# Kernel tuning notes

Hardware: AMD Instinct MI355X
Metric: run time of the kernel (lower is better)

The kernel has to match this reference:

```python
import jax, jax.numpy as jnp
import numpy as np

B, N = 8, 256
IN_F, OUT_F = 64, 64
IN_E, OUT_E = 32, 64  # out_edges must equal out_features (batched matmul constraint)


def setup_inputs() -> dict:
    key = jax.random.key(0)
    ks = jax.random.split(key, 9)
    s = 0.05
    return {
        "A": jax.random.uniform(ks[0], (B, N, N), dtype=jnp.float32),
        "emb_node": jax.random.normal(ks[1], (B, N, IN_F), dtype=jnp.float32),
        "emb_edge": jax.random.normal(ks[2], (B, N, N, IN_E), dtype=jnp.float32),
        "W_node": jax.random.normal(ks[3], (IN_F, OUT_F), dtype=jnp.float32) * s,
        "b_node": jnp.zeros((OUT_F,), dtype=jnp.float32),
        "W_nodes": jax.random.normal(ks[4], (IN_F, OUT_F), dtype=jnp.float32) * s,
        "b_nodes": jnp.zeros((OUT_F,), dtype=jnp.float32),
        "W_edge": jax.random.normal(ks[5], (IN_E, OUT_E), dtype=jnp.float32) * s,
        "b_edge": jnp.zeros((OUT_E,), dtype=jnp.float32),
    }


def reference(A, emb_node, emb_edge, W_node, b_node, W_nodes, b_nodes, W_edge, b_edge):
    # Dense projections (last-axis matmul, like keras Dense)
    node_x = emb_node @ W_node + b_node        # [B,N,F]
    node_sx = emb_node @ W_nodes + b_nodes     # [B,N,F]
    edge_x = emb_edge @ W_edge + b_edge        # [B,N,N,E] (E == F)
    # Fused edge-weighted aggregation: original materializes A[...,None]*edge_x
    # then does a per-channel batched matmul with node_x; same math as:
    #   node_out[b,n,f] = sum_m A[b,n,m] * edge_x[b,n,m,f] * node_x[b,m,f]
    agg = jnp.einsum('bnm,bnmf,bmf->bnf', A, edge_x, node_x)
    node_out = jax.nn.relu(agg) + jax.nn.relu(node_sx)
    edge_out = jax.nn.relu(edge_x)
    return node_out, edge_out
```

## Files before the change

kernel.cpp:

```cpp
#include <hip/hip_runtime.h>

#define BB    8
#define NN    256
#define OUTF  64
#define INE   32

using f4     = __attribute__((ext_vector_type(4))) float;
using f32x4  = __attribute__((ext_vector_type(4))) float;
using bf16x8 = __attribute__((ext_vector_type(8))) short;

__device__ float          g_node_x[BB * NN * OUTF];
__device__ float          g_relu_sx[BB * NN * OUTF];
__device__ unsigned short g_wtb[OUTF * INE];

static __device__ __forceinline__ unsigned short f2bf(float x) {
    unsigned u = __builtin_bit_cast(unsigned, x);
    u += 0x7fffu + ((u >> 16) & 1u);
    return (unsigned short)(u >> 16);
}

static __device__ __forceinline__ bf16x8 cvt8(f4 lo, f4 hi) {
    bf16x8 e;
    e[0] = (short)f2bf(lo.x); e[1] = (short)f2bf(lo.y);
    e[2] = (short)f2bf(lo.z); e[3] = (short)f2bf(lo.w);
    e[4] = (short)f2bf(hi.x); e[5] = (short)f2bf(hi.y);
    e[6] = (short)f2bf(hi.z); e[7] = (short)f2bf(hi.w);
    return e;
}

static __device__ __forceinline__ f4 relu4(f4 v) {
    f4 r;
    r.x = fmaxf(v.x, 0.f); r.y = fmaxf(v.y, 0.f);
    r.z = fmaxf(v.z, 0.f); r.w = fmaxf(v.w, 0.f);
    return r;
}

__global__ __launch_bounds__(256) void node_proj(
    const float* __restrict__ emb_node,
    const float* __restrict__ W1, const float* __restrict__ b1,
    const float* __restrict__ W2, const float* __restrict__ b2,
    const float* __restrict__ W_edge)
{
    __shared__ float sW1[64][64];
    __shared__ float sW2[64][64];
    __shared__ float sE[16][64];

    const int tid = threadIdx.x;

    if (blockIdx.x == 0) {
        const int f  = tid >> 2;
        const int k0 = (tid & 3) * 8;
#pragma unroll
        for (int j = 0; j < 8; ++j)
            g_wtb[f * INE + k0 + j] = f2bf(W_edge[(k0 + j) * OUTF + f]);
    }

    const f4* w1v = (const f4*)W1;
    const f4* w2v = (const f4*)W2;
    f4* s1 = (f4*)&sW1[0][0];
    f4* s2 = (f4*)&sW2[0][0];
#pragma unroll
    for (int i = 0; i < 4; ++i) {
        s1[tid + i * 256] = w1v[tid + i * 256];
        s2[tid + i * 256] = w2v[tid + i * 256];
    }
    const int row0 = blockIdx.x * 16;
    ((f4*)&sE[0][0])[tid] = ((const f4*)(emb_node + row0 * 64))[tid];
    __syncthreads();

    const int s = tid >> 6;
    const int f = tid & 63;
    float a1[4], a2[4];
    const float bb1 = b1[f], bb2 = b2[f];
#pragma unroll
    for (int j = 0; j < 4; ++j) { a1[j] = bb1; a2[j] = bb2; }
#pragma unroll
    for (int k = 0; k < 64; ++k) {
        const float w1 = sW1[k][f];
        const float w2 = sW2[k][f];
#pragma unroll
        for (int j = 0; j < 4; ++j) {
            const float e = sE[s + 4 * j][k];
            a1[j] = fmaf(e, w1, a1[j]);
            a2[j] = fmaf(e, w2, a2[j]);
        }
    }
#pragma unroll
    for (int j = 0; j < 4; ++j) {
        const int row = row0 + s + 4 * j;
        g_node_x[row * 64 + f]  = a1[j];
        g_relu_sx[row * 64 + f] = fmaxf(a2[j], 0.f);
    }
}

__global__ __launch_bounds__(256) void edge_agg(
    const float* __restrict__ A,
    const float* __restrict__ emb_edge,
    const float* __restrict__ b_edge,
    float* __restrict__ node_out,
    float* __restrict__ edge_out)
{
    __shared__ float sRed[4][64];

    const int tid  = threadIdx.x;
    const int bn   = blockIdx.x;
    const int b    = bn >> 8;
    const int wave = tid >> 6;
    const int lane = tid & 63;
    const int c    = lane & 15;
    const int q    = lane >> 4;
    const int wbase = wave * 64;

    bf16x8 wfrag[4];
    f4     bias[4];
#pragma unroll
    for (int ft = 0; ft < 4; ++ft) {
        wfrag[ft] = *(const bf16x8*)&g_wtb[(ft * 16 + c) * INE + q * 8];
        bias[ft]  = *(const f4*)&b_edge[ft * 16 + q * 4];
    }

    const float* ebase = emb_edge + (size_t)bn * (NN * INE);
    const float* Arow  = A + (size_t)bn * NN;
    const float* nx    = g_node_x + b * (NN * OUTF);
    float*       eo    = edge_out + (size_t)bn * (NN * OUTF);

    f4 agg[4];
#pragma unroll
    for (int ft = 0; ft < 4; ++ft) { agg[ft].x = 0.f; agg[ft].y = 0.f; agg[ft].z = 0.f; agg[ft].w = 0.f; }

    const float* rp0 = ebase + (wbase + c) * INE + q * 8;
    f4    plo = *(const f4*)rp0;
    f4    phi = *(const f4*)(rp0 + 4);
    float pa  = Arow[wbase + c];

#pragma unroll
    for (int mt = 0; mt < 4; ++mt) {
        const int m = wbase + mt * 16 + c;

        const f4    lo = plo;
        const f4    hi = phi;
        const float a  = pa;

        if (mt < 3) {
            const float* rpn = ebase + (m + 16) * INE + q * 8;
            plo = *(const f4*)rpn;
            phi = *(const f4*)(rpn + 4);
            pa  = Arow[m + 16];
        }

        const bf16x8 ef = cvt8(lo, hi);

        f32x4 acc[4];
#pragma unroll
        for (int ft = 0; ft < 4; ++ft)
            acc[ft] = __builtin_amdgcn_mfma_f32_16x16x32_bf16(
                wfrag[ft], ef, bias[ft], 0, 0, 0);

#pragma unroll
        for (int ft = 0; ft < 4; ++ft) {
            const int fb  = ft * 16 + q * 4;
            const f4  v   = acc[ft];
            const f4  nxv = *(const f4*)&nx[m * OUTF + fb];
            *(f4*)&eo[(size_t)m * OUTF + fb] = relu4(v);
            agg[ft].x = fmaf(a * v.x, nxv.x, agg[ft].x);
            agg[ft].y = fmaf(a * v.y, nxv.y, agg[ft].y);
            agg[ft].z = fmaf(a * v.z, nxv.z, agg[ft].z);
            agg[ft].w = fmaf(a * v.w, nxv.w, agg[ft].w);
        }

        __builtin_amdgcn_sched_barrier(0);
    }

#pragma unroll
    for (int ft = 0; ft < 4; ++ft) {
#pragma unroll
        for (int s = 1; s < 16; s <<= 1) {
            agg[ft].x += __shfl_xor(agg[ft].x, s);
            agg[ft].y += __shfl_xor(agg[ft].y, s);
            agg[ft].z += __shfl_xor(agg[ft].z, s);
            agg[ft].w += __shfl_xor(agg[ft].w, s);
        }
    }
    if (c == 0) {
#pragma unroll
        for (int ft = 0; ft < 4; ++ft)
            *(f4*)&sRed[wave][ft * 16 + q * 4] = agg[ft];
    }
    __syncthreads();

    if (tid < 64) {
        float s = sRed[0][tid] + sRed[1][tid] + sRed[2][tid] + sRed[3][tid];
        node_out[bn * OUTF + tid] = fmaxf(s, 0.f) + g_relu_sx[bn * OUTF + tid];
    }
}

extern "C" void kernel_launch(void* const* d_in, const int* in_sizes, int n_in,
                              void* d_out, int out_size, void* d_ws, size_t ws_size,
                              hipStream_t stream) {
    const float* A        = (const float*)d_in[0];
    const float* emb_node = (const float*)d_in[1];
    const float* emb_edge = (const float*)d_in[2];
    const float* W_node   = (const float*)d_in[3];
    const float* b_node   = (const float*)d_in[4];
    const float* W_nodes  = (const float*)d_in[5];
    const float* b_nodes  = (const float*)d_in[6];
    const float* W_edge   = (const float*)d_in[7];
    const float* b_edge   = (const float*)d_in[8];

    float* node_out = (float*)d_out;
    float* edge_out = node_out + BB * NN * OUTF;

    node_proj<<<(BB * NN) / 16, 256, 0, stream>>>(emb_node, W_node, b_node,
                                                  W_nodes, b_nodes, W_edge);
    edge_agg<<<BB * NN, 256, 0, stream>>>(A, emb_edge, b_edge, node_out, edge_out);
}
```

Baseline: 48.10 us.

## Stage edge weights, bias and A row in LDS and raise edge_agg occupancy

Weight fragments, bias and the A row are now loaded into shared memory once per block instead of being held in registers or read per lane from global memory. The MFMA loop is split into two halves of two feature tiles each, with a scheduling barrier after each half, to lower register pressure. Launch bounds now ask for 8 blocks per SM to raise occupancy. In exchange it adds a __syncthreads, LDS reads inside the inner loop, and possible spills under the tighter register budget.

```diff
diff --git a/kernel.cpp b/kernel.cpp
--- a/kernel.cpp
+++ b/kernel.cpp
@@ -93,13 +93,16 @@
     }
 }
 
-__global__ __launch_bounds__(256) void edge_agg(
+__global__ __launch_bounds__(256, 8) void edge_agg(
     const float* __restrict__ A,
     const float* __restrict__ emb_edge,
     const float* __restrict__ b_edge,
     float* __restrict__ node_out,
     float* __restrict__ edge_out)
 {
+    __shared__ unsigned short sWt[64 * 40];
+    __shared__ float sBias[64];
+    __shared__ float sA[256];
     __shared__ float sRed[4][64];
 
     const int tid  = threadIdx.x;
@@ -111,64 +114,74 @@
     const int q    = lane >> 4;
     const int wbase = wave * 64;
 
-    bf16x8 wfrag[4];
-    f4     bias[4];
-#pragma unroll
-    for (int ft = 0; ft < 4; ++ft) {
-        wfrag[ft] = *(const bf16x8*)&g_wtb[(ft * 16 + c) * INE + q * 8];
-        bias[ft]  = *(const f4*)&b_edge[ft * 16 + q * 4];
+    {
+        const f4 wv = *(const f4*)((const unsigned short*)g_wtb + tid * 8);
+        *(f4*)&sWt[(tid >> 2) * 40 + (tid & 3) * 8] = wv;
+        if (tid < 16) ((f4*)sBias)[tid] = ((const f4*)b_edge)[tid];
+        if (tid < 64) ((f4*)sA)[tid] = ((const f4*)(A + (size_t)bn * NN))[tid];
     }
 
     const float* ebase = emb_edge + (size_t)bn * (NN * INE);
-    const float* Arow  = A + (size_t)bn * NN;
     const float* nx    = g_node_x + b * (NN * OUTF);
     float*       eo    = edge_out + (size_t)bn * (NN * OUTF);
 
+    const float* rp0 = ebase + (wbase + c) * INE + q * 8;
+    f4 plo = *(const f4*)rp0;
+    f4 phi = *(const f4*)(rp0 + 4);
+
+    __syncthreads();
+
     f4 agg[4];
 #pragma unroll
     for (int ft = 0; ft < 4; ++ft) { agg[ft].x = 0.f; agg[ft].y = 0.f; agg[ft].z = 0.f; agg[ft].w = 0.f; }
-
-    const float* rp0 = ebase + (wbase + c) * INE + q * 8;
-    f4    plo = *(const f4*)rp0;
-    f4    phi = *(const f4*)(rp0 + 4);
-    float pa  = Arow[wbase + c];
 
 #pragma unroll
     for (int mt = 0; mt < 4; ++mt) {
         const int m = wbase + mt * 16 + c;
 
-        const f4    lo = plo;
-        const f4    hi = phi;
-        const float a  = pa;
-
+        const f4 lo = plo;
+        const f4 hi = phi;
         if (mt < 3) {
             const float* rpn = ebase + (m + 16) * INE + q * 8;
             plo = *(const f4*)rpn;
             phi = *(const f4*)(rpn + 4);
-            pa  = Arow[m + 16];
         }
 
         const bf16x8 ef = cvt8(lo, hi);
-
-        f32x4 acc[4];
-#pragma unroll
-        for (int ft = 0; ft < 4; ++ft)
-            acc[ft] = __builtin_amdgcn_mfma_f32_16x16x32_bf16(
-                wfrag[ft], ef, bias[ft], 0, 0, 0);
-
-#pragma unroll
-        for (int ft = 0; ft < 4; ++ft) {
-            const int fb  = ft * 16 + q * 4;
-            const f4  v   = acc[ft];
-            const f4  nxv = *(const f4*)&nx[m * OUTF + fb];
-            *(f4*)&eo[(size_t)m * OUTF + fb] = relu4(v);
-            agg[ft].x = fmaf(a * v.x, nxv.x, agg[ft].x);
-            agg[ft].y = fmaf(a * v.y, nxv.y, agg[ft].y);
-            agg[ft].z = fmaf(a * v.z, nxv.z, agg[ft].z);
-            agg[ft].w = fmaf(a * v.w, nxv.w, agg[ft].w);
-        }
-
-        __builtin_amdgcn_sched_barrier(0);
+        const float  a  = sA[m];
+
+#pragma unroll
+        for (int h = 0; h < 2; ++h) {
+            const int ftA = h * 2;
+            const int ftB = ftA + 1;
+            const bf16x8 wfA = *(const bf16x8*)&sWt[(ftA * 16 + c) * 40 + q * 8];
+            const bf16x8 wfB = *(const bf16x8*)&sWt[(ftB * 16 + c) * 40 + q * 8];
+            const f4     cbA = *(const f4*)&sBias[ftA * 16 + q * 4];
+            const f4     cbB = *(const f4*)&sBias[ftB * 16 + q * 4];
+
+            const f32x4 accA = __builtin_amdgcn_mfma_f32_16x16x32_bf16(wfA, ef, cbA, 0, 0, 0);
+            const f32x4 accB = __builtin_amdgcn_mfma_f32_16x16x32_bf16(wfB, ef, cbB, 0, 0, 0);
+
+            {
+                const int fb  = ftA * 16 + q * 4;
+                const f4  nxv = *(const f4*)&nx[m * OUTF + fb];
+                *(f4*)&eo[(size_t)m * OUTF + fb] = relu4(accA);
+                agg[ftA].x = fmaf(a * accA.x, nxv.x, agg[ftA].x);
+                agg[ftA].y = fmaf(a * accA.y, nxv.y, agg[ftA].y);
+                agg[ftA].z = fmaf(a * accA.z, nxv.z, agg[ftA].z);
+                agg[ftA].w = fmaf(a * accA.w, nxv.w, agg[ftA].w);
+            }
+            {
+                const int fb  = ftB * 16 + q * 4;
+                const f4  nxv = *(const f4*)&nx[m * OUTF + fb];
+                *(f4*)&eo[(size_t)m * OUTF + fb] = relu4(accB);
+                agg[ftB].x = fmaf(a * accB.x, nxv.x, agg[ftB].x);
+                agg[ftB].y = fmaf(a * accB.y, nxv.y, agg[ftB].y);
+                agg[ftB].z = fmaf(a * accB.z, nxv.z, agg[ftB].z);
+                agg[ftB].w = fmaf(a * accB.w, nxv.w, agg[ftB].w);
+            }
+            __builtin_amdgcn_sched_barrier(0);
+        }
     }
 
 #pragma unroll
```

New measurement: 167.6 us. +248.4%, slower.
